# Performance work log

Hardware: AMD Instinct MI355X
Metric: run time of the kernel (lower is better)

## Reference

```python
import jax, jax.numpy as jnp
import numpy as np

N_NODES = 50000
N_EDGES = 1250000
D_IN = 256
D_OUT = 64


def setup_inputs() -> dict:
    key = jax.random.key(0)
    k0, k1, k2, k3, k4 = jax.random.split(key, 5)
    return {
        "arg0_1": jax.random.normal(k0, (D_OUT, D_IN), dtype=jnp.float32),
        "arg1_1": jax.random.normal(k1, (D_OUT,), dtype=jnp.float32),
        "arg2_1": jax.random.randint(k2, (2, N_EDGES), 0, N_NODES, dtype=jnp.int64),
        "arg3_1": jax.random.uniform(k3, (N_EDGES,), dtype=jnp.float32),
        "arg4_1": jax.random.normal(k4, (N_NODES, D_IN), dtype=jnp.float32),
    }


def reference(arg0_1, arg1_1, arg2_1, arg3_1, arg4_1):
    # h = x @ W^T  : [N, D_OUT]
    h = jnp.matmul(arg4_1, arg0_1.T)
    src = arg2_1[0]  # gather indices
    dst = arg2_1[1]  # scatter_add indices
    # edge messages: gather source rows, scale by edge weight  : [E, D_OUT]
    msg = arg3_1[:, None] * h[src]
    # scatter_add into node buckets
    agg = jax.ops.segment_sum(msg, dst, num_segments=N_NODES)
    return agg + arg1_1
```

## Files before the change

### kernel.cpp

```cpp
#include <hip/hip_runtime.h>
#include <hip/hip_bf16.h>

#define D_IN    256
#define D_OUT   64
#define NNODES  50000
#define NEDGES  1250000

#define BUCK_SHIFT 7
#define BUCK_NODES 128
#define NBUCK      391
#define CPAD       16
#define EPB        4096
#define NB_EDGE    ((NEDGES + EPB - 1) / EPB)
#define GEMM_BLOCKS ((NNODES + 63) / 64)
#define BCAP    4092

typedef float f32x4 __attribute__((ext_vector_type(4)));
typedef short s16x8 __attribute__((ext_vector_type(8)));

static __device__ __forceinline__ unsigned short f2bf(float f) {
    union { float f; unsigned u; } v; v.f = f;
    unsigned r = v.u + 0x7FFFu + ((v.u >> 16) & 1u);
    return (unsigned short)(r >> 16);
}

__global__ __launch_bounds__(256) void gemm_bin(
    const float* __restrict__ x, const float* __restrict__ W,
    signed char* __restrict__ hq, float* __restrict__ scale_tab, int N,
    const int* __restrict__ src, const int* __restrict__ dst,
    const float* __restrict__ wt,
    int* __restrict__ bcursor, unsigned long long* __restrict__ binned)
{
    __shared__ uint4 sW[2048];
    __shared__ int   lcnt[NBUCK];
    __shared__ int   lbase[NBUCK];

    const int t = threadIdx.x;

    if (blockIdx.x >= GEMM_BLOCKS) {
        for (int i = t; i < NBUCK; i += 256) lcnt[i] = 0;
        __syncthreads();

        int base = (blockIdx.x - GEMM_BLOCKS) * EPB;
        bool full = (base + EPB <= NEDGES);

        if (full) {
            const int4* d4 = (const int4*)(dst + base);
            #pragma unroll
            for (int it = 0; it < 4; ++it) {
                int4 d = d4[t + it * 256];
                atomicAdd(&lcnt[d.x >> BUCK_SHIFT], 1);
                atomicAdd(&lcnt[d.y >> BUCK_SHIFT], 1);
                atomicAdd(&lcnt[d.z >> BUCK_SHIFT], 1);
                atomicAdd(&lcnt[d.w >> BUCK_SHIFT], 1);
            }
        } else {
            for (int e = base + t; e < NEDGES; e += 256)
                atomicAdd(&lcnt[dst[e] >> BUCK_SHIFT], 1);
        }
        __syncthreads();

        for (int i = t; i < NBUCK; i += 256) {
            int c = lcnt[i];
            lbase[i] = c ? (i * BCAP + atomicAdd(&bcursor[i * CPAD], c)) : 0;
            lcnt[i]  = 0;
        }
        __syncthreads();

        if (full) {
            const int4*   s4 = (const int4*)(src + base);
            const int4*   d4 = (const int4*)(dst + base);
            const float4* w4 = (const float4*)(wt + base);
            #pragma unroll
            for (int it = 0; it < 4; ++it) {
                int4   ss = s4[t + it * 256];
                int4   dd = d4[t + it * 256];
                float4 ww = w4[t + it * 256];
                int sv[4]   = {ss.x, ss.y, ss.z, ss.w};
                int dv[4]   = {dd.x, dd.y, dd.z, dd.w};
                float wv[4] = {ww.x, ww.y, ww.z, ww.w};
                #pragma unroll
                for (int k = 0; k < 4; ++k) {
                    int d = dv[k];
                    int b = d >> BUCK_SHIFT;
                    int r = atomicAdd(&lcnt[b], 1);
                    unsigned lo = (unsigned)sv[k] | ((unsigned)(d & (BUCK_NODES - 1)) << 16);
                    unsigned long long rec = (unsigned long long)lo
                                           | ((unsigned long long)__float_as_uint(wv[k]) << 32);
                    binned[lbase[b] + r] = rec;
                }
            }
        } else {
            for (int e = base + t; e < NEDGES; e += 256) {
                int d = dst[e];
                int b = d >> BUCK_SHIFT;
                int r = atomicAdd(&lcnt[b], 1);
                int sidx = src[e];
                unsigned lo = (unsigned)sidx | ((unsigned)(d & (BUCK_NODES - 1)) << 16);
                unsigned long long rec = (unsigned long long)lo
                                       | ((unsigned long long)__float_as_uint(wt[e]) << 32);
                binned[lbase[b] + r] = rec;
            }
        }
        return;
    }

    const int lane = t & 63;
    const int wave = t >> 6;
    const int m    = lane & 15;
    const int q    = lane >> 4;

    #pragma unroll
    for (int i = 0; i < 8; ++i) {
        int slot = t + i * 256;
        int ln   = slot & 63;
        int kb   = (slot >> 6) & 7;
        int c    = slot >> 9;
        int lm = ln & 15, lq = ln >> 4;
        const float* wp = W + (c * 16 + lm) * D_IN + kb * 32 + lq * 8;
        float4 w0 = *(const float4*)wp;
        float4 w1 = *(const float4*)(wp + 4);
        uint4 u;
        u.x = (unsigned)f2bf(w0.x) | ((unsigned)f2bf(w0.y) << 16);
        u.y = (unsigned)f2bf(w0.z) | ((unsigned)f2bf(w0.w) << 16);
        u.z = (unsigned)f2bf(w1.x) | ((unsigned)f2bf(w1.y) << 16);
        u.w = (unsigned)f2bf(w1.z) | ((unsigned)f2bf(w1.w) << 16);
        sW[slot] = u;
    }
    __syncthreads();

    const int rowA = blockIdx.x * 64 + wave * 16 + m;
    const int rowc = (rowA < N) ? rowA : (N - 1);
    const float* xr = x + (long long)rowc * D_IN + q * 8;

    f32x4 acc[4] = {};

    #pragma unroll
    for (int kb = 0; kb < 8; ++kb) {
        float4 a0 = *(const float4*)(xr + kb * 32);
        float4 a1 = *(const float4*)(xr + kb * 32 + 4);
        s16x8 af;
        af[0] = (short)f2bf(a0.x); af[1] = (short)f2bf(a0.y);
        af[2] = (short)f2bf(a0.z); af[3] = (short)f2bf(a0.w);
        af[4] = (short)f2bf(a1.x); af[5] = (short)f2bf(a1.y);
        af[6] = (short)f2bf(a1.z); af[7] = (short)f2bf(a1.w);

        #pragma unroll
        for (int c = 0; c < 4; ++c) {
            s16x8 bf = *(const s16x8*)&sW[(c * 8 + kb) * 64 + lane];
            acc[c] = __builtin_amdgcn_mfma_f32_16x16x32_bf16(af, bf, acc[c], 0, 0, 0);
        }
    }

    #pragma unroll
    for (int r = 0; r < 4; ++r) {
        float local = fmaxf(fmaxf(fabsf(acc[0][r]), fabsf(acc[1][r])),
                            fmaxf(fabsf(acc[2][r]), fabsf(acc[3][r])));
        #pragma unroll
        for (int msk = 1; msk < 16; msk <<= 1)
            local = fmaxf(local, __shfl_xor(local, msk));
        float amax = fmaxf(local, 1e-6f);
        float inv  = 127.0f / amax;
        int gr = blockIdx.x * 64 + wave * 16 + q * 4 + r;
        if (gr < N) {
            if (m == 0) scale_tab[gr] = amax * (1.0f / 127.0f);
            #pragma unroll
            for (int c = 0; c < 4; ++c) {
                int qv = __float2int_rn(acc[c][r] * inv);
                hq[(long long)gr * D_OUT + c * 16 + m] = (signed char)qv;
            }
        }
    }
}

__global__ __launch_bounds__(512) void sortagg(
    const unsigned long long* __restrict__ binned, const int* __restrict__ bcursor,
    const float* __restrict__ scale_tab, const signed char* __restrict__ hq,
    const float* __restrict__ bias, float* __restrict__ out)
{
    __shared__ unsigned long long srt[BCAP];
    __shared__ int s[256];
    __shared__ int lcnt[BUCK_NODES];
    __shared__ int lstart[BUCK_NODES];
    __shared__ int lcur[BUCK_NODES];
    const int t = threadIdx.x;
    const int b = blockIdx.x;

    const unsigned long long* bsrc = binned + (long long)b * BCAP;
    unsigned long long rv[8];
    #pragma unroll
    for (int j = 0; j < 8; ++j) {
        int k = t + j * 512;
        rv[j] = (k < BCAP) ? bsrc[k] : 0ULL;
    }

    const int cntb = bcursor[b * CPAD];
    if (t < BUCK_NODES) lcnt[t] = 0;
    __syncthreads();

    #pragma unroll
    for (int j = 0; j < 8; ++j) {
        int k = t + j * 512;
        if (k < cntb)
            atomicAdd(&lcnt[(int)((rv[j] >> 16) & 0xFF)], 1);
    }
    __syncthreads();

    int v2 = 0;
    if (t < 256) { v2 = (t < BUCK_NODES) ? lcnt[t] : 0; s[t] = v2; }
    __syncthreads();
    #pragma unroll
    for (int off = 1; off < 256; off <<= 1) {
        int u = (t < 256 && t >= off) ? s[t - off] : 0;
        __syncthreads();
        if (t < 256) s[t] += u;
        __syncthreads();
    }
    if (t < BUCK_NODES) {
        int excl = s[t] - v2;
        lstart[t] = excl;
        lcur[t]   = excl;
    }
    __syncthreads();

    #pragma unroll
    for (int j = 0; j < 8; ++j) {
        int k = t + j * 512;
        if (k < cntb) {
            unsigned long long r = rv[j];
            int dloc = (int)((r >> 16) & 0xFF);
            int sidx = (int)(r & 0xFFFF);
            float wf = __uint_as_float((unsigned)(r >> 32)) * scale_tab[sidx];
            int pos  = atomicAdd(&lcur[dloc], 1);
            srt[pos] = (r & 0xFFFFFFFFull)
                     | ((unsigned long long)__float_as_uint(wf) << 32);
        }
    }
    __syncthreads();

    const int lane  = t & 63;
    const int wave  = t >> 6;
    const int node0 = b << BUCK_SHIFT;
    const int nn    = min(BUCK_NODES, NNODES - node0);
    const float bv  = bias[lane];

    for (int jj = 0; jj < 16; ++jj) {
        int n = wave * 16 + jj;
        if (n >= nn) break;
        float acc = 0.0f;
        int st  = lstart[n];
        int cnt = lcnt[n];
        int i = st, e = st + cnt;

        for (; i + 7 < e; i += 8) {
            unsigned long long q0 = srt[i + 0];
            unsigned long long q1 = srt[i + 1];
            unsigned long long q2 = srt[i + 2];
            unsigned long long q3 = srt[i + 3];
            unsigned long long q4 = srt[i + 4];
            unsigned long long q5 = srt[i + 5];
            unsigned long long q6 = srt[i + 6];
            unsigned long long q7 = srt[i + 7];
            float v0 = (float)hq[(int)(q0 & 0xFFFF) * D_OUT + lane];
            float v1 = (float)hq[(int)(q1 & 0xFFFF) * D_OUT + lane];
            float v2_ = (float)hq[(int)(q2 & 0xFFFF) * D_OUT + lane];
            float v3 = (float)hq[(int)(q3 & 0xFFFF) * D_OUT + lane];
            float v4 = (float)hq[(int)(q4 & 0xFFFF) * D_OUT + lane];
            float v5 = (float)hq[(int)(q5 & 0xFFFF) * D_OUT + lane];
            float v6 = (float)hq[(int)(q6 & 0xFFFF) * D_OUT + lane];
            float v7 = (float)hq[(int)(q7 & 0xFFFF) * D_OUT + lane];
            acc += __uint_as_float((unsigned)(q0 >> 32)) * v0;
            acc += __uint_as_float((unsigned)(q1 >> 32)) * v1;
            acc += __uint_as_float((unsigned)(q2 >> 32)) * v2_;
            acc += __uint_as_float((unsigned)(q3 >> 32)) * v3;
            acc += __uint_as_float((unsigned)(q4 >> 32)) * v4;
            acc += __uint_as_float((unsigned)(q5 >> 32)) * v5;
            acc += __uint_as_float((unsigned)(q6 >> 32)) * v6;
            acc += __uint_as_float((unsigned)(q7 >> 32)) * v7;
        }
        for (; i + 3 < e; i += 4) {
            unsigned long long q0 = srt[i + 0];
            unsigned long long q1 = srt[i + 1];
            unsigned long long q2 = srt[i + 2];
            unsigned long long q3 = srt[i + 3];
            float v0 = (float)hq[(int)(q0 & 0xFFFF) * D_OUT + lane];
            float v1 = (float)hq[(int)(q1 & 0xFFFF) * D_OUT + lane];
            float v2_ = (float)hq[(int)(q2 & 0xFFFF) * D_OUT + lane];
            float v3 = (float)hq[(int)(q3 & 0xFFFF) * D_OUT + lane];
            acc += __uint_as_float((unsigned)(q0 >> 32)) * v0;
            acc += __uint_as_float((unsigned)(q1 >> 32)) * v1;
            acc += __uint_as_float((unsigned)(q2 >> 32)) * v2_;
            acc += __uint_as_float((unsigned)(q3 >> 32)) * v3;
        }
        for (; i < e; ++i) {
            unsigned long long q = srt[i];
            acc += __uint_as_float((unsigned)(q >> 32))
                 * (float)hq[(int)(q & 0xFFFF) * D_OUT + lane];
        }
        out[(long long)(node0 + n) * D_OUT + lane] = acc + bv;
    }
}

__global__ __launch_bounds__(256) void init_bias(
    float* __restrict__ out, const float* __restrict__ bias, int total)
{
    int i = blockIdx.x * blockDim.x + threadIdx.x;
    if (i < total) out[i] = bias[i & (D_OUT - 1)];
}

__global__ __launch_bounds__(256) void scatter_edges(
    const int* __restrict__ src, const int* __restrict__ dst,
    const float* __restrict__ wt, const signed char* __restrict__ hq,
    const float* __restrict__ scale_tab, float* __restrict__ out)
{
    long long gid = (long long)blockIdx.x * blockDim.x + threadIdx.x;
    int e    = (int)(gid >> 6);
    int lane = threadIdx.x & 63;
    if (e < NEDGES) {
        int   s = src[e];
        int   d = dst[e];
        float w = wt[e] * scale_tab[s];
        float v = w * (float)hq[(long long)s * D_OUT + lane];
        atomicAdd(&out[(long long)d * D_OUT + lane], v);
    }
}

extern "C" void kernel_launch(void* const* d_in, const int* in_sizes, int n_in,
                              void* d_out, int out_size, void* d_ws, size_t ws_size,
                              hipStream_t stream)
{
    const float* W     = (const float*)d_in[0];
    const float* bias  = (const float*)d_in[1];
    const int*   edges = (const int*)  d_in[2];
    const float* wt    = (const float*)d_in[3];
    const float* x     = (const float*)d_in[4];
    float*       out   = (float*)d_out;

    const int* src = edges;
    const int* dst = edges + NEDGES;

    char* ws = (char*)d_ws;
    const size_t OFF_HQ     = 0;
    const size_t OFF_SCALE  = 3200000;
    const size_t OFF_BCUR   = 3400000;
    const size_t REQUIRED   = 3425024;

    signed char* hq        = (signed char*)(ws + OFF_HQ);
    float*       scale_tab = (float*)(ws + OFF_SCALE);

    if (ws_size >= REQUIRED) {
        int* bcursor = (int*)(ws + OFF_BCUR);

        unsigned long long* binned = (unsigned long long*)d_out;

        hipMemsetAsync(bcursor, 0, NBUCK * CPAD * sizeof(int), stream);

        gemm_bin<<<GEMM_BLOCKS + NB_EDGE, 256, 0, stream>>>(
            x, W, hq, scale_tab, NNODES, src, dst, wt, bcursor, binned);

        sortagg<<<NBUCK, 512, 0, stream>>>(binned, bcursor, scale_tab,
                                           hq, bias, out);
    } else {
        gemm_bin<<<GEMM_BLOCKS, 256, 0, stream>>>(
            x, W, hq, scale_tab, NNODES,
            (const int*)nullptr, (const int*)nullptr, (const float*)nullptr,
            (int*)nullptr, (unsigned long long*)nullptr);
        int total = NNODES * D_OUT;
        init_bias<<<(total + 255) / 256, 256, 0, stream>>>(out, bias, total);
        long long threads = (long long)NEDGES * 64;
        int blocks = (int)((threads + 255) / 256);
        scatter_edges<<<blocks, 256, 0, stream>>>(src, dst, wt, hq, scale_tab, out);
    }
}
```

Measured before the change: 168.9 us.

## Stage binned edge records in shared memory sorted by bucket before global write

For full edge chunks, the binning blocks now load src, dst and weight once into registers instead of reading dst twice. They build a per-block prefix scan over bucket counts and scatter records into a shared-memory array sorted by bucket. That array is then copied to global memory, so each bucket's records go out as a contiguous run rather than as scattered 8-byte stores. The full dst index is now stored in the record, and the consumer masks it with 0x7F. Shared memory is unioned with the GEMM weight tile, and the change adds an extra scan and several barriers per binning block.

```diff
diff --git a/kernel.cpp b/kernel.cpp
--- a/kernel.cpp
+++ b/kernel.cpp
@@ -31,75 +31,115 @@
     const float* __restrict__ wt,
     int* __restrict__ bcursor, unsigned long long* __restrict__ binned)
 {
-    __shared__ uint4 sW[2048];
-    __shared__ int   lcnt[NBUCK];
-    __shared__ int   lbase[NBUCK];
+    __shared__ union {
+        uint4 sW[2048];
+        struct {
+            unsigned long long srt[EPB];
+            int s[256];
+            int lcnt[NBUCK];
+            int lbase[NBUCK];
+            int lstartL[NBUCK];
+        } bin;
+    } sh;
 
     const int t = threadIdx.x;
 
     if (blockIdx.x >= GEMM_BLOCKS) {
-        for (int i = t; i < NBUCK; i += 256) lcnt[i] = 0;
+        for (int i = t; i < NBUCK; i += 256) sh.bin.lcnt[i] = 0;
         __syncthreads();
 
         int base = (blockIdx.x - GEMM_BLOCKS) * EPB;
         bool full = (base + EPB <= NEDGES);
 
         if (full) {
-            const int4* d4 = (const int4*)(dst + base);
+            int4 dd[4], ss[4]; float4 ww[4];
+            const int4*   d4 = (const int4*)(dst + base);
+            const int4*   s4 = (const int4*)(src + base);
+            const float4* w4 = (const float4*)(wt + base);
             #pragma unroll
             for (int it = 0; it < 4; ++it) {
-                int4 d = d4[t + it * 256];
-                atomicAdd(&lcnt[d.x >> BUCK_SHIFT], 1);
-                atomicAdd(&lcnt[d.y >> BUCK_SHIFT], 1);
-                atomicAdd(&lcnt[d.z >> BUCK_SHIFT], 1);
-                atomicAdd(&lcnt[d.w >> BUCK_SHIFT], 1);
-            }
-        } else {
-            for (int e = base + t; e < NEDGES; e += 256)
-                atomicAdd(&lcnt[dst[e] >> BUCK_SHIFT], 1);
-        }
-        __syncthreads();
-
-        for (int i = t; i < NBUCK; i += 256) {
-            int c = lcnt[i];
-            lbase[i] = c ? (i * BCAP + atomicAdd(&bcursor[i * CPAD], c)) : 0;
-            lcnt[i]  = 0;
-        }
-        __syncthreads();
-
-        if (full) {
-            const int4*   s4 = (const int4*)(src + base);
-            const int4*   d4 = (const int4*)(dst + base);
-            const float4* w4 = (const float4*)(wt + base);
+                dd[it] = d4[t + it * 256];
+                ss[it] = s4[t + it * 256];
+                ww[it] = w4[t + it * 256];
+            }
+
             #pragma unroll
             for (int it = 0; it < 4; ++it) {
-                int4   ss = s4[t + it * 256];
-                int4   dd = d4[t + it * 256];
-                float4 ww = w4[t + it * 256];
-                int sv[4]   = {ss.x, ss.y, ss.z, ss.w};
-                int dv[4]   = {dd.x, dd.y, dd.z, dd.w};
-                float wv[4] = {ww.x, ww.y, ww.z, ww.w};
+                atomicAdd(&sh.bin.lcnt[dd[it].x >> BUCK_SHIFT], 1);
+                atomicAdd(&sh.bin.lcnt[dd[it].y >> BUCK_SHIFT], 1);
+                atomicAdd(&sh.bin.lcnt[dd[it].z >> BUCK_SHIFT], 1);
+                atomicAdd(&sh.bin.lcnt[dd[it].w >> BUCK_SHIFT], 1);
+            }
+            __syncthreads();
+
+            int i0 = 2 * t, i1 = 2 * t + 1;
+            int v0 = (i0 < NBUCK) ? sh.bin.lcnt[i0] : 0;
+            int v1 = (i1 < NBUCK) ? sh.bin.lcnt[i1] : 0;
+            sh.bin.s[t] = v0 + v1;
+            __syncthreads();
+            #pragma unroll
+            for (int off = 1; off < 256; off <<= 1) {
+                int u = (t >= off) ? sh.bin.s[t - off] : 0;
+                __syncthreads();
+                sh.bin.s[t] += u;
+                __syncthreads();
+            }
+            int excl = sh.bin.s[t] - (v0 + v1);
+            if (i0 < NBUCK) sh.bin.lstartL[i0] = excl;
+            if (i1 < NBUCK) sh.bin.lstartL[i1] = excl + v0;
+            __syncthreads();
+
+            for (int i = t; i < NBUCK; i += 256) {
+                int c = sh.bin.lcnt[i];
+                sh.bin.lbase[i] = c ? (i * BCAP + atomicAdd(&bcursor[i * CPAD], c)) : 0;
+                sh.bin.lcnt[i] = 0;
+            }
+            __syncthreads();
+
+            #pragma unroll
+            for (int it = 0; it < 4; ++it) {
+                int dv[4]   = {dd[it].x, dd[it].y, dd[it].z, dd[it].w};
+                int sv[4]   = {ss[it].x, ss[it].y, ss[it].z, ss[it].w};
+                float wv[4] = {ww[it].x, ww[it].y, ww[it].z, ww[it].w};
                 #pragma unroll
                 for (int k = 0; k < 4; ++k) {
                     int d = dv[k];
                     int b = d >> BUCK_SHIFT;
-                    int r = atomicAdd(&lcnt[b], 1);
-                    unsigned lo = (unsigned)sv[k] | ((unsigned)(d & (BUCK_NODES - 1)) << 16);
-                    unsigned long long rec = (unsigned long long)lo
-                                           | ((unsigned long long)__float_as_uint(wv[k]) << 32);
-                    binned[lbase[b] + r] = rec;
+                    int r = atomicAdd(&sh.bin.lcnt[b], 1);
+                    unsigned lo = (unsigned)sv[k] | ((unsigned)d << 16);
+                    sh.bin.srt[sh.bin.lstartL[b] + r] =
+                        (unsigned long long)lo
+                        | ((unsigned long long)__float_as_uint(wv[k]) << 32);
                 }
             }
+            __syncthreads();
+
+            #pragma unroll
+            for (int it = 0; it < 16; ++it) {
+                int i = t + it * 256;
+                unsigned long long rec = sh.bin.srt[i];
+                int d = (int)((rec >> 16) & 0xFFFF);
+                int b = d >> BUCK_SHIFT;
+                binned[sh.bin.lbase[b] + (i - sh.bin.lstartL[b])] = rec;
+            }
         } else {
+            for (int e = base + t; e < NEDGES; e += 256)
+                atomicAdd(&sh.bin.lcnt[dst[e] >> BUCK_SHIFT], 1);
+            __syncthreads();
+            for (int i = t; i < NBUCK; i += 256) {
+                int c = sh.bin.lcnt[i];
+                sh.bin.lbase[i] = c ? (i * BCAP + atomicAdd(&bcursor[i * CPAD], c)) : 0;
+                sh.bin.lcnt[i] = 0;
+            }
+            __syncthreads();
             for (int e = base + t; e < NEDGES; e += 256) {
                 int d = dst[e];
                 int b = d >> BUCK_SHIFT;
-                int r = atomicAdd(&lcnt[b], 1);
-                int sidx = src[e];
-                unsigned lo = (unsigned)sidx | ((unsigned)(d & (BUCK_NODES - 1)) << 16);
-                unsigned long long rec = (unsigned long long)lo
-                                       | ((unsigned long long)__float_as_uint(wt[e]) << 32);
-                binned[lbase[b] + r] = rec;
+                int r = atomicAdd(&sh.bin.lcnt[b], 1);
+                unsigned lo = (unsigned)src[e] | ((unsigned)d << 16);
+                binned[sh.bin.lbase[b] + r] =
+                    (unsigned long long)lo
+                    | ((unsigned long long)__float_as_uint(wt[e]) << 32);
             }
         }
         return;
@@ -125,7 +165,7 @@
         u.y = (unsigned)f2bf(w0.z) | ((unsigned)f2bf(w0.w) << 16);
         u.z = (unsigned)f2bf(w1.x) | ((unsigned)f2bf(w1.y) << 16);
         u.w = (unsigned)f2bf(w1.z) | ((unsigned)f2bf(w1.w) << 16);
-        sW[slot] = u;
+        sh.sW[slot] = u;
     }
     __syncthreads();
 
@@ -147,7 +187,7 @@
 
         #pragma unroll
         for (int c = 0; c < 4; ++c) {
-            s16x8 bf = *(const s16x8*)&sW[(c * 8 + kb) * 64 + lane];
+            s16x8 bf = *(const s16x8*)&sh.sW[(c * 8 + kb) * 64 + lane];
             acc[c] = __builtin_amdgcn_mfma_f32_16x16x32_bf16(af, bf, acc[c], 0, 0, 0);
         }
     }
@@ -202,7 +242,7 @@
     for (int j = 0; j < 8; ++j) {
         int k = t + j * 512;
         if (k < cntb)
-            atomicAdd(&lcnt[(int)((rv[j] >> 16) & 0xFF)], 1);
+            atomicAdd(&lcnt[(int)((rv[j] >> 16) & 0x7F)], 1);
     }
     __syncthreads();
 
@@ -228,7 +268,7 @@
         int k = t + j * 512;
         if (k < cntb) {
             unsigned long long r = rv[j];
-            int dloc = (int)((r >> 16) & 0xFF);
+            int dloc = (int)((r >> 16) & 0x7F);
             int sidx = (int)(r & 0xFFFF);
             float wf = __uint_as_float((unsigned)(r >> 32)) * scale_tab[sidx];
             int pos  = atomicAdd(&lcur[dloc], 1);
```

Result: faster. 154.9 us (-8.3%).
